# Performance work log

Measured on AMD Instinct MI355X. Metric: run time of the kernel, lower is better.

## Reference

```python
import jax, jax.numpy as jnp
import numpy as np

N_NODES = 500_000
N_EDGES = 8_000_000
N_GRAPHS = 5_000
CHANNELS = 8
CONVS = 8
HIDDEN = 128
NODE_TYPES = 6
EPS = 1e-5


def setup_inputs() -> dict:
    key = jax.random.key(0)
    ks = jax.random.split(key, 12)
    x = jax.random.randint(ks[0], (N_NODES,), 0, NODE_TYPES, dtype=jnp.int64 if jax.config.jax_enable_x64 else jnp.int32)
    edge_index = jax.random.randint(ks[1], (2, N_EDGES), 0, N_NODES, dtype=jnp.int32)
    batch = jax.random.randint(ks[2], (N_NODES,), 0, N_GRAPHS, dtype=jnp.int32)
    emb = jax.random.normal(ks[3], (NODE_TYPES, CHANNELS), jnp.float32)
    bn_gamma = jnp.ones((CONVS, CHANNELS), jnp.float32)
    bn_beta = jnp.zeros((CONVS, CHANNELS), jnp.float32)
    conv_w = jax.random.normal(ks[4], (CONVS, CHANNELS, CHANNELS), jnp.float32) / np.sqrt(CHANNELS)
    conv_b = jnp.zeros((CONVS, CHANNELS), jnp.float32)
    hid_w = jax.random.normal(ks[5], (CHANNELS, HIDDEN), jnp.float32) / np.sqrt(CHANNELS)
    hid_b = jnp.zeros((HIDDEN,), jnp.float32)
    out_w = jax.random.normal(ks[6], (HIDDEN, 1), jnp.float32) / np.sqrt(HIDDEN)
    out_b = jnp.zeros((1,), jnp.float32)
    return {"x": x, "edge_index": edge_index, "batch": batch, "emb": emb,
            "bn_gamma": bn_gamma, "bn_beta": bn_beta, "conv_w": conv_w, "conv_b": conv_b,
            "hid_w": hid_w, "hid_b": hid_b, "out_w": out_w, "out_b": out_b}


def reference(x, edge_index, batch, emb, bn_gamma, bn_beta, conv_w, conv_b,
              hid_w, hid_b, out_w, out_b):
    # GCNConv norm with self-loops (PyG defaults: add_self_loops=True, normalize=True)
    loop = jnp.arange(N_NODES, dtype=edge_index.dtype)
    src = jnp.concatenate([edge_index[0], loop])  # [E+N]
    dst = jnp.concatenate([edge_index[1], loop])
    deg = jax.ops.segment_sum(jnp.ones_like(src, jnp.float32), dst, num_segments=N_NODES)
    dinv = jax.lax.rsqrt(deg)  # deg >= 1 due to self-loops
    norm = (dinv[src] * dinv[dst])[:, None]  # [E+N, 1]

    h = emb[x]  # [N, C]
    for i in range(CONVS):
        # BatchNorm (training-mode batch statistics over nodes)
        mu = h.mean(axis=0)
        var = h.var(axis=0)
        hb = (h - mu) * jax.lax.rsqrt(var + EPS) * bn_gamma[i] + bn_beta[i]
        # GCNConv: linear transform then normalized scatter-add aggregation
        hw = hb @ conv_w[i]  # [N, C]
        agg = jax.ops.segment_sum(norm * hw[src], dst, num_segments=N_NODES) + conv_b[i]
        h = jax.nn.relu(h + agg)  # residual + relu

    pooled = jax.ops.segment_sum(h, batch, num_segments=N_GRAPHS)  # [G, C]
    hid = jax.nn.relu(pooled @ hid_w + hid_b)  # [G, HIDDEN]
    return (hid @ out_w + out_b).squeeze(-1)  # [G]
```

## Files before the change

### kernel.cpp

```cpp
#include <hip/hip_runtime.h>

#define NN 500000
#define NE 8000000
#define NG 5000
#define CH 8
#define NCONV 8
#define HID 128
#define BEPS 1e-5f

#define NBLK 1954
#define NBLK2 15625

#define NWIN 512
#define WNODE 977
#define WCAP 18432
#define PCHUNK 16384
#define NPBLK ((NE + PCHUNK - 1) / PCHUNK)

static inline size_t alignup(size_t v, size_t a) { return (v + a - 1) / a * a; }

__global__ void k_init(int* __restrict__ wcur, double* __restrict__ pooled) {
    int i = blockIdx.x * 256 + threadIdx.x;
    if (i < NWIN) wcur[i] = 0;
    if (i < NG * CH) pooled[i] = 0.0;
}

__global__ void __launch_bounds__(1024) k_part(const int* __restrict__ src,
                                               const int* __restrict__ dst,
                                               int* __restrict__ wcur,
                                               unsigned int* __restrict__ bucket) {
    __shared__ int cnt[NWIN], base[NWIN], lcur[NWIN];
    int tid = threadIdx.x;
    for (int i = tid; i < NWIN; i += 1024) cnt[i] = 0;
    __syncthreads();
    int start = blockIdx.x * PCHUNK;
#pragma unroll
    for (int k = 0; k < PCHUNK / 1024; k++) {
        int e = start + k * 1024 + tid;
        if (e < NE) atomicAdd(&cnt[dst[e] / WNODE], 1);
    }
    __syncthreads();
    for (int i = tid; i < NWIN; i += 1024) {
        base[i] = atomicAdd(&wcur[i], cnt[i]);
        lcur[i] = 0;
    }
    __syncthreads();
#pragma unroll
    for (int k = 0; k < PCHUNK / 1024; k++) {
        int e = start + k * 1024 + tid;
        if (e < NE) {
            int d = dst[e];
            int s = src[e];
            int w = d / WNODE;
            int p = base[w] + atomicAdd(&lcur[w], 1);
            if (p < WCAP)
                bucket[(size_t)w * WCAP + p] = ((unsigned)(d - w * WNODE) << 19) | (unsigned)s;
        }
    }
}

__global__ void k_wscan(const int* __restrict__ wcur, int* __restrict__ wbase,
                        int* __restrict__ rowptr) {
    __shared__ int s[NWIN];
    int tid = threadIdx.x;
    int v = wcur[tid]; if (v > WCAP) v = WCAP;
    s[tid] = v;
    __syncthreads();
    for (int off = 1; off < NWIN; off <<= 1) {
        int t = (tid >= off) ? s[tid - off] : 0;
        __syncthreads();
        s[tid] += t;
        __syncthreads();
    }
    wbase[tid] = s[tid] - v;
    if (tid == NWIN - 1) rowptr[NN] = s[tid];
}

__global__ void __launch_bounds__(1024) k_sortwin(const int* __restrict__ wcur,
                                                  const int* __restrict__ wbase,
                                                  const unsigned int* __restrict__ bucket,
                                                  int* __restrict__ rowptr,
                                                  float* __restrict__ dinv,
                                                  float* __restrict__ dsq,
                                                  int* __restrict__ csr) {
    __shared__ int lh[WNODE];
    __shared__ unsigned int sout[WCAP];
    __shared__ int wsums[16];
    int w = blockIdx.x, tid = threadIdx.x;
    int n = wcur[w]; if (n > WCAP) n = WCAP;
    const unsigned int* bp = bucket + (size_t)w * WCAP;
    for (int i = tid; i < WNODE; i += 1024) lh[i] = 0;
    __syncthreads();
    for (int e = tid; e < n; e += 1024)
        atomicAdd(&lh[__builtin_nontemporal_load(bp + e) >> 19], 1);
    __syncthreads();
    int gbase = w * WNODE;
    int nnode = NN - gbase; if (nnode > WNODE) nnode = WNODE;
    int v = (tid < WNODE) ? lh[tid] : 0;
    int lane = tid & 63, wid = tid >> 6;
    int incl = v;
#pragma unroll
    for (int off = 1; off < 64; off <<= 1) {
        int t = __shfl_up(incl, off);
        if (lane >= off) incl += t;
    }
    if (lane == 63) wsums[wid] = incl;
    __syncthreads();
    if (tid == 0) {
        int run = 0;
#pragma unroll
        for (int i = 0; i < 16; i++) { int t = wsums[i]; wsums[i] = run; run += t; }
    }
    __syncthreads();
    int excl = incl - v + wsums[wid];
    if (tid < nnode) {
        rowptr[gbase + tid] = wbase[w] + excl;
        float deg = (float)(v + 1);
        dinv[gbase + tid] = rsqrtf(deg);
        dsq[gbase + tid] = sqrtf(deg);
    }
    __syncthreads();
    if (tid < WNODE) lh[tid] = excl;
    __syncthreads();
    for (int e = tid; e < n; e += 1024) {
        unsigned int p = __builtin_nontemporal_load(bp + e);
        int pos = atomicAdd(&lh[p >> 19], 1);
        sout[pos] = p & 0x7FFFFu;
    }
    __syncthreads();
    int cb = wbase[w];
    for (int e = tid; e < n; e += 1024)
        csr[cb + e] = (int)sout[e];
}

__global__ void k_s1(const int* __restrict__ rowptr, const int* __restrict__ csr,
                     const float* __restrict__ dinv, float* __restrict__ S1) {
    int n = blockIdx.x * 256 + threadIdx.x;
    if (n >= NN) return;
    int beg = rowptr[n], end = rowptr[n + 1];
    double a = 0.0;
    for (int e = beg; e < end; e++) a += (double)dinv[__builtin_nontemporal_load(csr + e)];
    S1[n] = (float)a;
}

__global__ void k_rstats(const float* __restrict__ partial, int nblk, double* __restrict__ stats) {
    int slot = blockIdx.x;
    int tid = threadIdx.x;
    double acc = 0.0;
    for (int j = tid; j < nblk; j += 256) acc += (double)partial[(size_t)j * 16 + slot];
#pragma unroll
    for (int off = 32; off; off >>= 1) acc += __shfl_xor(acc, off);
    __shared__ double ls[4];
    if ((tid & 63) == 0) ls[tid >> 6] = acc;
    __syncthreads();
    if (tid == 0) stats[slot] = ls[0] + ls[1] + ls[2] + ls[3];
}

__device__ __forceinline__ void block_stats_accum(const float v[CH], float* __restrict__ partial) {
    __shared__ float ls[4][2 * CH];
    int tid = threadIdx.x;
#pragma unroll
    for (int c = 0; c < CH; c++) {
        float s = v[c], q = v[c] * v[c];
#pragma unroll
        for (int off = 32; off; off >>= 1) {
            s += __shfl_xor(s, off);
            q += __shfl_xor(q, off);
        }
        if ((tid & 63) == 0) {
            ls[tid >> 6][c] = s;
            ls[tid >> 6][CH + c] = q;
        }
    }
    __syncthreads();
    if (tid < 2 * CH)
        partial[(size_t)blockIdx.x * 2 * CH + tid] =
            ls[0][tid] + ls[1][tid] + ls[2][tid] + ls[3][tid];
}

__global__ void k_embed(const int* __restrict__ x, const float* __restrict__ emb,
                        const float* __restrict__ dinv,
                        float* __restrict__ hsc, float* __restrict__ partial) {
    int i = blockIdx.x * 256 + threadIdx.x;
    float v[CH];
    if (i < NN) {
        int t = x[i];
#pragma unroll
        for (int c = 0; c < CH; c++) v[c] = emb[t * CH + c];
        float d = dinv[i];
        float4* hp = (float4*)(hsc + (size_t)i * CH);
        hp[0] = make_float4(v[0] * d, v[1] * d, v[2] * d, v[3] * d);
        hp[1] = make_float4(v[4] * d, v[5] * d, v[6] * d, v[7] * d);
    } else {
#pragma unroll
        for (int c = 0; c < CH; c++) v[c] = 0.0f;
    }
    block_stats_accum(v, partial);
}

__device__ __forceinline__ float conv_val(const int* __restrict__ rowptr,
                                          const int* __restrict__ csr,
                                          const float* __restrict__ dinv,
                                          const float* __restrict__ dsq,
                                          const float* __restrict__ S1,
                                          const float* __restrict__ hsc_in,
                                          const float* sW, const float* sScale,
                                          const float* sShift, const float* sBias,
                                          int t, int node, int c) {
    int beg = rowptr[node], end = rowptr[node + 1];
    double acc0 = 0.0, acc1 = 0.0;
    int e = beg;
    for (; e + 3 < end; e += 4) {
        int s0 = __builtin_nontemporal_load(csr + e);
        int s1 = __builtin_nontemporal_load(csr + e + 1);
        int s2 = __builtin_nontemporal_load(csr + e + 2);
        int s3 = __builtin_nontemporal_load(csr + e + 3);
        acc0 += (double)hsc_in[(size_t)s0 * CH + c] + (double)hsc_in[(size_t)s1 * CH + c];
        acc1 += (double)hsc_in[(size_t)s2 * CH + c] + (double)hsc_in[(size_t)s3 * CH + c];
    }
    for (; e < end; e++)
        acc0 += (double)hsc_in[(size_t)__builtin_nontemporal_load(csr + e) * CH + c];
    float self = hsc_in[t];
    float pre = (float)(acc0 + acc1 + (double)self);
    float d = dinv[node];
    float s1tot = S1[node] + d;
    float pc = pre * sScale[c] + s1tot * sShift[c];
    int base = (threadIdx.x & 63) & ~7;
    float o = 0.0f;
#pragma unroll
    for (int k = 0; k < 8; k++) o += __shfl(pc, base + k) * sW[k * CH + c];
    return self * dsq[node] + sBias[c] + d * o;
}

__device__ __forceinline__ void load_layer_params(const double* __restrict__ stats,
                                                  const float* __restrict__ gamma,
                                                  const float* __restrict__ beta,
                                                  const float* __restrict__ W,
                                                  const float* __restrict__ bias,
                                                  float* sW, float* sScale,
                                                  float* sShift, float* sBias) {
    int tid = threadIdx.x;
    if (tid < CH * CH) sW[tid] = W[tid];
    if (tid < CH) {
        double mu = stats[tid] * (1.0 / NN);
        double var = stats[CH + tid] * (1.0 / NN) - mu * mu;
        float sc = gamma[tid] * rsqrtf((float)var + BEPS);
        sScale[tid] = sc;
        sShift[tid] = beta[tid] - (float)mu * sc;
        sBias[tid] = bias[tid];
    }
    __syncthreads();
}

__global__ void __launch_bounds__(256) k_gconv(const int* __restrict__ rowptr,
                                               const int* __restrict__ csr,
                                               const float* __restrict__ dinv,
                                               const float* __restrict__ dsq,
                                               const float* __restrict__ S1,
                                               const double* __restrict__ stats,
                                               const float* __restrict__ gamma,
                                               const float* __restrict__ beta,
                                               const float* __restrict__ W,
                                               const float* __restrict__ bias,
                                               const float* __restrict__ hsc_in,
                                               float* __restrict__ hsc_out,
                                               float* __restrict__ partial) {
    __shared__ float sW[CH * CH], sScale[CH], sShift[CH], sBias[CH];
    load_layer_params(stats, gamma, beta, W, bias, sW, sScale, sShift, sBias);
    int t = blockIdx.x * 256 + threadIdx.x;
    int node = t >> 3, c = t & 7;
    float val = conv_val(rowptr, csr, dinv, dsq, S1, hsc_in, sW, sScale, sShift, sBias,
                         t, node, c);
    float v = fmaxf(val, 0.0f);
    hsc_out[t] = v * dinv[node];
    float s = v, q = v * v;
#pragma unroll
    for (int off = 8; off < 64; off <<= 1) {
        s += __shfl_xor(s, off);
        q += __shfl_xor(q, off);
    }
    __shared__ float ls[4][2 * CH];
    int lane = threadIdx.x & 63, wid = threadIdx.x >> 6;
    if (lane < CH) { ls[wid][lane] = s; ls[wid][CH + lane] = q; }
    __syncthreads();
    if (threadIdx.x < 2 * CH)
        partial[(size_t)blockIdx.x * 2 * CH + threadIdx.x] =
            ls[0][threadIdx.x] + ls[1][threadIdx.x] + ls[2][threadIdx.x] + ls[3][threadIdx.x];
}

__global__ void __launch_bounds__(256) k_gpool(const int* __restrict__ rowptr,
                                               const int* __restrict__ csr,
                                               const float* __restrict__ dinv,
                                               const float* __restrict__ dsq,
                                               const float* __restrict__ S1,
                                               const double* __restrict__ stats,
                                               const float* __restrict__ gamma,
                                               const float* __restrict__ beta,
                                               const float* __restrict__ W,
                                               const float* __restrict__ bias,
                                               const float* __restrict__ hsc_in,
                                               const int* __restrict__ batch,
                                               double* __restrict__ pooled) {
    __shared__ float sW[CH * CH], sScale[CH], sShift[CH], sBias[CH];
    load_layer_params(stats, gamma, beta, W, bias, sW, sScale, sShift, sBias);
    int t = blockIdx.x * 256 + threadIdx.x;
    int node = t >> 3, c = t & 7;
    float val = conv_val(rowptr, csr, dinv, dsq, S1, hsc_in, sW, sScale, sShift, sBias,
                         t, node, c);
    atomicAdd(&pooled[(size_t)batch[node] * CH + c], (double)fmaxf(val, 0.0f));
}

__global__ void k_mlp(const double* __restrict__ pooled, const float* __restrict__ hid_w,
                      const float* __restrict__ hid_b, const float* __restrict__ out_w,
                      const float* __restrict__ out_b, float* __restrict__ out) {
    int g = blockIdx.x;
    int j = threadIdx.x;
    __shared__ float sp[CH];
    __shared__ float part[2];
    if (j < CH) sp[j] = (float)pooled[(size_t)g * CH + j];
    __syncthreads();
    float acc = hid_b[j];
#pragma unroll
    for (int c = 0; c < CH; c++) acc += sp[c] * hid_w[c * HID + j];
    acc = fmaxf(acc, 0.0f) * out_w[j];
#pragma unroll
    for (int off = 32; off; off >>= 1) acc += __shfl_xor(acc, off);
    if ((j & 63) == 0) part[j >> 6] = acc;
    __syncthreads();
    if (j == 0) out[g] = part[0] + part[1] + out_b[0];
}

extern "C" void kernel_launch(void* const* d_in, const int* in_sizes, int n_in,
                              void* d_out, int out_size, void* d_ws, size_t ws_size,
                              hipStream_t stream) {
    const int* x = (const int*)d_in[0];
    const int* ei = (const int*)d_in[1];
    const int* srcp = ei;
    const int* dstp = ei + NE;
    const int* batch = (const int*)d_in[2];
    const float* emb = (const float*)d_in[3];
    const float* gamma = (const float*)d_in[4];
    const float* beta = (const float*)d_in[5];
    const float* convw = (const float*)d_in[6];
    const float* convb = (const float*)d_in[7];
    const float* hid_w = (const float*)d_in[8];
    const float* hid_b = (const float*)d_in[9];
    const float* out_w = (const float*)d_in[10];
    const float* out_b = (const float*)d_in[11];
    float* out = (float*)d_out;

    char* ws = (char*)d_ws;
    size_t off = 0;
    int*   rowptr  = (int*)(ws + off);   off = alignup(off + ((size_t)NN + 1) * 4, 256);
    float* dinv    = (float*)(ws + off); off = alignup(off + (size_t)NN * 4, 256);
    float* dsq     = (float*)(ws + off); off = alignup(off + (size_t)NN * 4, 256);
    float* S1      = (float*)(ws + off); off = alignup(off + (size_t)NN * 4, 256);
    int*   wcur    = (int*)(ws + off);   off = alignup(off + NWIN * 4, 256);
    int*   wbase   = (int*)(ws + off);   off = alignup(off + NWIN * 4, 256);
    int*   csr     = (int*)(ws + off);   off = alignup(off + (size_t)NE * 4, 256);
    double* pooled = (double*)(ws + off); off = alignup(off + (size_t)NG * CH * 8, 256);
    float* partial = (float*)(ws + off); off = alignup(off + (size_t)NBLK2 * 2 * CH * 4, 256);
    double* stats  = (double*)(ws + off); off = alignup(off + 2 * CH * 8, 256);
    unsigned int* bucket = (unsigned int*)(ws + off);
    float* hA      = (float*)(ws + off);
    float* hB      = (float*)(ws + off + alignup((size_t)NN * CH * 4, 256));

    const int B = 256;

    k_init<<<(NG * CH + B - 1) / B, B, 0, stream>>>(wcur, pooled);
    k_part<<<NPBLK, 1024, 0, stream>>>(srcp, dstp, wcur, bucket);
    k_wscan<<<1, NWIN, 0, stream>>>(wcur, wbase, rowptr);
    k_sortwin<<<NWIN, 1024, 0, stream>>>(wcur, wbase, bucket, rowptr, dinv, dsq, csr);
    k_s1<<<NBLK, B, 0, stream>>>(rowptr, csr, dinv, S1);
    k_embed<<<NBLK, B, 0, stream>>>(x, emb, dinv, hA, partial);
    k_rstats<<<16, 256, 0, stream>>>(partial, NBLK, stats);

    float* hc = hA;
    float* hn = hB;
    for (int i = 0; i < NCONV; i++) {
        if (i < NCONV - 1) {
            k_gconv<<<NBLK2, B, 0, stream>>>(rowptr, csr, dinv, dsq, S1, stats,
                                             gamma + i * CH, beta + i * CH,
                                             convw + i * CH * CH, convb + i * CH,
                                             hc, hn, partial);
            k_rstats<<<16, 256, 0, stream>>>(partial, NBLK2, stats);
            float* tmp = hc; hc = hn; hn = tmp;
        } else {
            k_gpool<<<NBLK2, B, 0, stream>>>(rowptr, csr, dinv, dsq, S1, stats,
                                             gamma + i * CH, beta + i * CH,
                                             convw + i * CH * CH, convb + i * CH,
                                             hc, batch, pooled);
        }
    }
    k_mlp<<<NG, HID, 0, stream>>>(pooled, hid_w, hid_b, out_w, out_b, out);
}
```

Measured before the change: 1.548 ms.

## Sort CSR by source window and sweep windows with grid-synchronized persistent conv kernel

The CSR build now orders each destination's neighbor list by source window (8 windows of 62,500 nodes), and the conv kernel becomes a persistent grid of 256×1024 threads. Each 8-thread group handles 16 nodes. All blocks step through the source windows in lockstep using a spin barrier in global memory, which bounded-timeouts after a fixed budget. The aim is to keep the gathered feature rows of the current window resident in cache instead of random-gathering across the whole 16MB feature array. The cost is fewer threads, serialized per-slot loops with data-dependent breaks, and a barrier that assumes all 256 blocks are co-resident.

```diff
diff --git a/kernel.cpp b/kernel.cpp
--- a/kernel.cpp
+++ b/kernel.cpp
@@ -9,20 +9,28 @@
 #define BEPS 1e-5f
 
 #define NBLK 1954
-#define NBLK2 15625
 
 #define NWIN 512
 #define WNODE 977
 #define WCAP 18432
 #define PCHUNK 16384
 #define NPBLK ((NE + PCHUNK - 1) / PCHUNK)
+#define SWIN 8
+#define SWNODE 62500
+
+#define GBLK 256
+#define GTHR 1024
+#define NGRP (GBLK * GTHR / 8)
+#define NSLOT 16
 
 static inline size_t alignup(size_t v, size_t a) { return (v + a - 1) / a * a; }
 
-__global__ void k_init(int* __restrict__ wcur, double* __restrict__ pooled) {
+__global__ void k_init(int* __restrict__ wcur, double* __restrict__ pooled,
+                       int* __restrict__ bar) {
     int i = blockIdx.x * 256 + threadIdx.x;
     if (i < NWIN) wcur[i] = 0;
     if (i < NG * CH) pooled[i] = 0.0;
+    if (i < NCONV * (SWIN - 1)) bar[i] = 0;
 }
 
 __global__ void __launch_bounds__(1024) k_part(const int* __restrict__ src,
@@ -83,22 +91,32 @@
                                                   float* __restrict__ dinv,
                                                   float* __restrict__ dsq,
                                                   int* __restrict__ csr) {
-    __shared__ int lh[WNODE];
+    __shared__ int lh[WNODE * SWIN];
     __shared__ unsigned int sout[WCAP];
     __shared__ int wsums[16];
     int w = blockIdx.x, tid = threadIdx.x;
     int n = wcur[w]; if (n > WCAP) n = WCAP;
     const unsigned int* bp = bucket + (size_t)w * WCAP;
-    for (int i = tid; i < WNODE; i += 1024) lh[i] = 0;
-    __syncthreads();
-    for (int e = tid; e < n; e += 1024)
-        atomicAdd(&lh[__builtin_nontemporal_load(bp + e) >> 19], 1);
+    for (int i = tid; i < WNODE * SWIN; i += 1024) lh[i] = 0;
+    __syncthreads();
+    for (int e = tid; e < n; e += 1024) {
+        unsigned int p = __builtin_nontemporal_load(bp + e);
+        int bin = (int)(p >> 19) * SWIN + (int)(p & 0x7FFFFu) / SWNODE;
+        atomicAdd(&lh[bin], 1);
+    }
     __syncthreads();
     int gbase = w * WNODE;
     int nnode = NN - gbase; if (nnode > WNODE) nnode = WNODE;
-    int v = (tid < WNODE) ? lh[tid] : 0;
+    int v[SWIN]; int tot = 0;
+    if (tid < WNODE) {
+#pragma unroll
+        for (int k = 0; k < SWIN; k++) { v[k] = lh[tid * SWIN + k]; tot += v[k]; }
+    } else {
+#pragma unroll
+        for (int k = 0; k < SWIN; k++) v[k] = 0;
+    }
     int lane = tid & 63, wid = tid >> 6;
-    int incl = v;
+    int incl = tot;
 #pragma unroll
     for (int off = 1; off < 64; off <<= 1) {
         int t = __shfl_up(incl, off);
@@ -112,20 +130,25 @@
         for (int i = 0; i < 16; i++) { int t = wsums[i]; wsums[i] = run; run += t; }
     }
     __syncthreads();
-    int excl = incl - v + wsums[wid];
+    int excl = incl - tot + wsums[wid];
     if (tid < nnode) {
         rowptr[gbase + tid] = wbase[w] + excl;
-        float deg = (float)(v + 1);
+        float deg = (float)(tot + 1);
         dinv[gbase + tid] = rsqrtf(deg);
         dsq[gbase + tid] = sqrtf(deg);
     }
-    __syncthreads();
-    if (tid < WNODE) lh[tid] = excl;
+    if (tid < WNODE) {
+        int run = excl;
+#pragma unroll
+        for (int k = 0; k < SWIN; k++) { lh[tid * SWIN + k] = run; run += v[k]; }
+    }
     __syncthreads();
     for (int e = tid; e < n; e += 1024) {
         unsigned int p = __builtin_nontemporal_load(bp + e);
-        int pos = atomicAdd(&lh[p >> 19], 1);
-        sout[pos] = p & 0x7FFFFu;
+        int srcv = (int)(p & 0x7FFFFu);
+        int bin = (int)(p >> 19) * SWIN + srcv / SWNODE;
+        int pos = atomicAdd(&lh[bin], 1);
+        sout[pos] = (unsigned)srcv;
     }
     __syncthreads();
     int cb = wbase[w];
@@ -139,7 +162,7 @@
     if (n >= NN) return;
     int beg = rowptr[n], end = rowptr[n + 1];
     double a = 0.0;
-    for (int e = beg; e < end; e++) a += (double)dinv[__builtin_nontemporal_load(csr + e)];
+    for (int e = beg; e < end; e++) a += (double)dinv[csr[e]];
     S1[n] = (float)a;
 }
 
@@ -196,40 +219,6 @@
         for (int c = 0; c < CH; c++) v[c] = 0.0f;
     }
     block_stats_accum(v, partial);
-}
-
-__device__ __forceinline__ float conv_val(const int* __restrict__ rowptr,
-                                          const int* __restrict__ csr,
-                                          const float* __restrict__ dinv,
-                                          const float* __restrict__ dsq,
-                                          const float* __restrict__ S1,
-                                          const float* __restrict__ hsc_in,
-                                          const float* sW, const float* sScale,
-                                          const float* sShift, const float* sBias,
-                                          int t, int node, int c) {
-    int beg = rowptr[node], end = rowptr[node + 1];
-    double acc0 = 0.0, acc1 = 0.0;
-    int e = beg;
-    for (; e + 3 < end; e += 4) {
-        int s0 = __builtin_nontemporal_load(csr + e);
-        int s1 = __builtin_nontemporal_load(csr + e + 1);
-        int s2 = __builtin_nontemporal_load(csr + e + 2);
-        int s3 = __builtin_nontemporal_load(csr + e + 3);
-        acc0 += (double)hsc_in[(size_t)s0 * CH + c] + (double)hsc_in[(size_t)s1 * CH + c];
-        acc1 += (double)hsc_in[(size_t)s2 * CH + c] + (double)hsc_in[(size_t)s3 * CH + c];
-    }
-    for (; e < end; e++)
-        acc0 += (double)hsc_in[(size_t)__builtin_nontemporal_load(csr + e) * CH + c];
-    float self = hsc_in[t];
-    float pre = (float)(acc0 + acc1 + (double)self);
-    float d = dinv[node];
-    float s1tot = S1[node] + d;
-    float pc = pre * sScale[c] + s1tot * sShift[c];
-    int base = (threadIdx.x & 63) & ~7;
-    float o = 0.0f;
-#pragma unroll
-    for (int k = 0; k < 8; k++) o += __shfl(pc, base + k) * sW[k * CH + c];
-    return self * dsq[node] + sBias[c] + d * o;
 }
 
 __device__ __forceinline__ void load_layer_params(const double* __restrict__ stats,
@@ -252,62 +241,106 @@
     __syncthreads();
 }
 
-__global__ void __launch_bounds__(256) k_gconv(const int* __restrict__ rowptr,
-                                               const int* __restrict__ csr,
-                                               const float* __restrict__ dinv,
-                                               const float* __restrict__ dsq,
-                                               const float* __restrict__ S1,
-                                               const double* __restrict__ stats,
-                                               const float* __restrict__ gamma,
-                                               const float* __restrict__ beta,
-                                               const float* __restrict__ W,
-                                               const float* __restrict__ bias,
-                                               const float* __restrict__ hsc_in,
-                                               float* __restrict__ hsc_out,
-                                               float* __restrict__ partial) {
+template <bool POOL>
+__global__ void __launch_bounds__(GTHR) k_gphase(const int* __restrict__ rowptr,
+                                                 const int* __restrict__ csr,
+                                                 const float* __restrict__ dinv,
+                                                 const float* __restrict__ dsq,
+                                                 const float* __restrict__ S1,
+                                                 const double* __restrict__ stats,
+                                                 const float* __restrict__ gamma,
+                                                 const float* __restrict__ beta,
+                                                 const float* __restrict__ W,
+                                                 const float* __restrict__ bias,
+                                                 const float* __restrict__ hsc_in,
+                                                 float* __restrict__ hsc_out,
+                                                 const int* __restrict__ batch,
+                                                 double* __restrict__ pooled,
+                                                 float* __restrict__ partial,
+                                                 int* __restrict__ bar, int bslot) {
     __shared__ float sW[CH * CH], sScale[CH], sShift[CH], sBias[CH];
     load_layer_params(stats, gamma, beta, W, bias, sW, sScale, sShift, sBias);
-    int t = blockIdx.x * 256 + threadIdx.x;
-    int node = t >> 3, c = t & 7;
-    float val = conv_val(rowptr, csr, dinv, dsq, S1, hsc_in, sW, sScale, sShift, sBias,
-                         t, node, c);
-    float v = fmaxf(val, 0.0f);
-    hsc_out[t] = v * dinv[node];
-    float s = v, q = v * v;
-#pragma unroll
-    for (int off = 8; off < 64; off <<= 1) {
-        s += __shfl_xor(s, off);
-        q += __shfl_xor(q, off);
-    }
-    __shared__ float ls[4][2 * CH];
-    int lane = threadIdx.x & 63, wid = threadIdx.x >> 6;
-    if (lane < CH) { ls[wid][lane] = s; ls[wid][CH + lane] = q; }
-    __syncthreads();
-    if (threadIdx.x < 2 * CH)
-        partial[(size_t)blockIdx.x * 2 * CH + threadIdx.x] =
-            ls[0][threadIdx.x] + ls[1][threadIdx.x] + ls[2][threadIdx.x] + ls[3][threadIdx.x];
-}
-
-__global__ void __launch_bounds__(256) k_gpool(const int* __restrict__ rowptr,
-                                               const int* __restrict__ csr,
-                                               const float* __restrict__ dinv,
-                                               const float* __restrict__ dsq,
-                                               const float* __restrict__ S1,
-                                               const double* __restrict__ stats,
-                                               const float* __restrict__ gamma,
-                                               const float* __restrict__ beta,
-                                               const float* __restrict__ W,
-                                               const float* __restrict__ bias,
-                                               const float* __restrict__ hsc_in,
-                                               const int* __restrict__ batch,
-                                               double* __restrict__ pooled) {
-    __shared__ float sW[CH * CH], sScale[CH], sShift[CH], sBias[CH];
-    load_layer_params(stats, gamma, beta, W, bias, sW, sScale, sShift, sBias);
-    int t = blockIdx.x * 256 + threadIdx.x;
-    int node = t >> 3, c = t & 7;
-    float val = conv_val(rowptr, csr, dinv, dsq, S1, hsc_in, sW, sScale, sShift, sBias,
-                         t, node, c);
-    atomicAdd(&pooled[(size_t)batch[node] * CH + c], (double)fmaxf(val, 0.0f));
+    int tid = threadIdx.x;
+    int g = (blockIdx.x * GTHR + tid) >> 3;
+    int c = tid & 7;
+    int n0 = g * NSLOT;
+    int cur[NSLOT], end_[NSLOT];
+    double acc[NSLOT];
+#pragma unroll
+    for (int s = 0; s < NSLOT; s++) {
+        int node = n0 + s;
+        if (node < NN) { cur[s] = rowptr[node]; end_[s] = rowptr[node + 1]; }
+        else { cur[s] = 0; end_[s] = 0; }
+        acc[s] = 0.0;
+    }
+    for (int w = 0; w < SWIN; w++) {
+        int lim = (w + 1) * SWNODE;
+#pragma unroll
+        for (int s = 0; s < NSLOT; s++) {
+            int e = cur[s], en = end_[s];
+            double a = acc[s];
+            while (e < en) {
+                int srcv = csr[e];
+                if (srcv >= lim) break;
+                a += (double)hsc_in[(size_t)srcv * CH + c];
+                e++;
+            }
+            cur[s] = e; acc[s] = a;
+        }
+        if (w < SWIN - 1) {
+            __syncthreads();
+            if (tid == 0) {
+                int idx = bslot + w;
+                __hip_atomic_fetch_add(&bar[idx], 1, __ATOMIC_RELAXED, __HIP_MEMORY_SCOPE_AGENT);
+                int budget = 4000;
+                while (__hip_atomic_load(&bar[idx], __ATOMIC_RELAXED, __HIP_MEMORY_SCOPE_AGENT) < GBLK
+                       && --budget) {}
+            }
+            __syncthreads();
+        }
+    }
+    float sv = 0.0f, qv = 0.0f;
+#pragma unroll
+    for (int s = 0; s < NSLOT; s++) {
+        int node = n0 + s;
+        bool act = node < NN;
+        float self = act ? hsc_in[(size_t)node * CH + c] : 0.0f;
+        float d = act ? dinv[node] : 0.0f;
+        float s1t = act ? (S1[node] + d) : 0.0f;
+        float pre = (float)(acc[s] + (double)self);
+        float pc = pre * sScale[c] + s1t * sShift[c];
+        int base = (tid & 63) & ~7;
+        float o = 0.0f;
+#pragma unroll
+        for (int k = 0; k < 8; k++) o += __shfl(pc, base + k) * sW[k * CH + c];
+        if (act) {
+            float val = self * dsq[node] + sBias[c] + d * o;
+            float v = fmaxf(val, 0.0f);
+            if (POOL) {
+                atomicAdd(&pooled[(size_t)batch[node] * CH + c], (double)v);
+            } else {
+                hsc_out[(size_t)node * CH + c] = v * d;
+                sv += v; qv += v * v;
+            }
+        }
+    }
+    if (!POOL) {
+#pragma unroll
+        for (int off = 8; off < 64; off <<= 1) {
+            sv += __shfl_xor(sv, off);
+            qv += __shfl_xor(qv, off);
+        }
+        __shared__ float ls[16][2 * CH];
+        int lane = tid & 63, wid = tid >> 6;
+        if (lane < CH) { ls[wid][lane] = sv; ls[wid][CH + lane] = qv; }
+        __syncthreads();
+        if (tid < 2 * CH) {
+            float a = 0.0f;
+#pragma unroll
+            for (int i = 0; i < 16; i++) a += ls[i][tid];
+            partial[(size_t)blockIdx.x * 2 * CH + tid] = a;
+        }
+    }
 }
 
 __global__ void k_mlp(const double* __restrict__ pooled, const float* __restrict__ hid_w,
@@ -357,9 +390,10 @@
     float* S1      = (float*)(ws + off); off = alignup(off + (size_t)NN * 4, 256);
     int*   wcur    = (int*)(ws + off);   off = alignup(off + NWIN * 4, 256);
     int*   wbase   = (int*)(ws + off);   off = alignup(off + NWIN * 4, 256);
+    int*   bar     = (int*)(ws + off);   off = alignup(off + NCONV * (SWIN - 1) * 4, 256);
     int*   csr     = (int*)(ws + off);   off = alignup(off + (size_t)NE * 4, 256);
     double* pooled = (double*)(ws + off); off = alignup(off + (size_t)NG * CH * 8, 256);
-    float* partial = (float*)(ws + off); off = alignup(off + (size_t)NBLK2 * 2 * CH * 4, 256);
+    float* partial = (float*)(ws + off); off = alignup(off + (size_t)NBLK * 2 * CH * 4, 256);
     double* stats  = (double*)(ws + off); off = alignup(off + 2 * CH * 8, 256);
     unsigned int* bucket = (unsigned int*)(ws + off);
     float* hA      = (float*)(ws + off);
@@ -367,7 +401,7 @@
 
     const int B = 256;
 
-    k_init<<<(NG * CH + B - 1) / B, B, 0, stream>>>(wcur, pooled);
+    k_init<<<(NG * CH + B - 1) / B, B, 0, stream>>>(wcur, pooled, bar);
     k_part<<<NPBLK, 1024, 0, stream>>>(srcp, dstp, wcur, bucket);
     k_wscan<<<1, NWIN, 0, stream>>>(wcur, wbase, rowptr);
     k_sortwin<<<NWIN, 1024, 0, stream>>>(wcur, wbase, bucket, rowptr, dinv, dsq, csr);
@@ -378,18 +412,21 @@
     float* hc = hA;
     float* hn = hB;
     for (int i = 0; i < NCONV; i++) {
+        int bslot = i * (SWIN - 1);
         if (i < NCONV - 1) {
-            k_gconv<<<NBLK2, B, 0, stream>>>(rowptr, csr, dinv, dsq, S1, stats,
-                                             gamma + i * CH, beta + i * CH,
-                                             convw + i * CH * CH, convb + i * CH,
-                                             hc, hn, partial);
-            k_rstats<<<16, 256, 0, stream>>>(partial, NBLK2, stats);
+            k_gphase<false><<<GBLK, GTHR, 0, stream>>>(rowptr, csr, dinv, dsq, S1, stats,
+                                                       gamma + i * CH, beta + i * CH,
+                                                       convw + i * CH * CH, convb + i * CH,
+                                                       hc, hn, batch, pooled, partial,
+                                                       bar, bslot);
+            k_rstats<<<16, 256, 0, stream>>>(partial, GBLK, stats);
             float* tmp = hc; hc = hn; hn = tmp;
         } else {
-            k_gpool<<<NBLK2, B, 0, stream>>>(rowptr, csr, dinv, dsq, S1, stats,
-                                             gamma + i * CH, beta + i * CH,
-                                             convw + i * CH * CH, convb + i * CH,
-                                             hc, batch, pooled);
+            k_gphase<true><<<GBLK, GTHR, 0, stream>>>(rowptr, csr, dinv, dsq, S1, stats,
+                                                      gamma + i * CH, beta + i * CH,
+                                                      convw + i * CH * CH, convb + i * CH,
+                                                      hc, (float*)nullptr, batch, pooled, partial,
+                                                      bar, bslot);
         }
     }
     k_mlp<<<NG, HID, 0, stream>>>(pooled, hid_w, hid_b, out_w, out_b, out);
```

After: 3.717 ms. 140% more time.
